# Performance work log

Hardware: AMD Instinct MI355X
Metric: run time of the kernel (lower is better)

## Reference

```python
import jax, jax.numpy as jnp
import numpy as np

NUM_ITERATIONS = 10
ALPHA = 0.1


def setup_inputs() -> dict:
    key = jax.random.key(0)
    k1, k2, k3, k4 = jax.random.split(key, 4)
    N, E, F_IN, H = 100000, 3200000, 512, 64
    x = jax.random.normal(k1, (N, F_IN), dtype=jnp.float32)
    edge_index = jax.random.randint(k2, (2, E), 0, N, dtype=jnp.int32)
    edge_weight = jnp.ones((E,), dtype=jnp.float32)
    # glorot-ish scaled dense weights
    W0 = jax.random.normal(k3, (F_IN, H), dtype=jnp.float32) * (2.0 / (F_IN + H)) ** 0.5
    b0 = jnp.zeros((H,), dtype=jnp.float32)
    W1 = jax.random.normal(k4, (H, H), dtype=jnp.float32) * (2.0 / (H + H)) ** 0.5
    b1 = jnp.zeros((H,), dtype=jnp.float32)
    return {"x": x, "edge_index": edge_index, "edge_weight": edge_weight,
            "W0": W0, "b0": b0, "W1": W1, "b1": b1}


def _gcn_norm_edge(edge_index, edge_weight, num_nodes):
    # renorm: add self-loops with weight 1, then symmetric D^-1/2 A D^-1/2
    row, col = edge_index[0], edge_index[1]
    loop = jnp.arange(num_nodes, dtype=edge_index.dtype)
    row = jnp.concatenate([row, loop])
    col = jnp.concatenate([col, loop])
    w = jnp.concatenate([edge_weight, jnp.ones((num_nodes,), edge_weight.dtype)])
    deg = jax.ops.segment_sum(w, row, num_segments=num_nodes)
    dinv = jnp.where(deg > 0, jax.lax.rsqrt(jnp.where(deg > 0, deg, 1.0)), 0.0)
    w_norm = dinv[row] * w * dinv[col]
    return row, col, w_norm


def reference(x, edge_index, edge_weight, W0, b0, W1, b1):
    N = x.shape[0]
    # MLP: hidden layers relu-activated, last layer unactivated
    h = jax.nn.relu(x @ W0 + b0)
    h = h @ W1 + b1  # [N, H]

    row, col, w_norm = _gcn_norm_edge(edge_index, edge_weight, N)

    def step(z, _):
        # sparse propagation: gather at source, weight, scatter-add at dest
        msg = z[row] * w_norm[:, None]                      # [E+N, H]
        agg = jax.ops.segment_sum(msg, col, num_segments=N)  # [N, H]
        return (1.0 - ALPHA) * agg + ALPHA * h, None

    z, _ = jax.lax.scan(step, h, None, length=NUM_ITERATIONS)
    return z
```

## Files before the change

### kernel.cpp

```cpp
#include <hip/hip_runtime.h>


#define PAGE 16128
#define BPP 64
#define XST 136

typedef __attribute__((ext_vector_type(8))) short bf16x8;
typedef __attribute__((ext_vector_type(4))) float f32x4;

__device__ __forceinline__ float bf_lo(unsigned z) { return __uint_as_float(z << 16); }
__device__ __forceinline__ float bf_hi(unsigned z) { return __uint_as_float(z & 0xffff0000u); }
__device__ __forceinline__ unsigned bf_rne(float x) {
    unsigned u = __float_as_uint(x);
    return (u + 0x7fffu + ((u >> 16) & 1u)) >> 16;
}
__device__ __forceinline__ unsigned bf_pack(float x, float y) { return bf_rne(x) | (bf_rne(y) << 16); }

__global__ __launch_bounds__(256) void k_deg(const int* __restrict__ row, const float* __restrict__ ew,
                                             float* __restrict__ slab, int E, int chunk) {
    __shared__ float hf[PAGE];
    int p = blockIdx.x / BPP, b = blockIdx.x - p * BPP;
    int lo = p * PAGE;
    for (int i = threadIdx.x; i < PAGE; i += 256) hf[i] = 0.f;
    __syncthreads();
    int e0 = b * chunk, e1 = min(e0 + chunk, E);
    int evec = e0 + ((e1 - e0) & ~3);
    for (int e = e0 + (int)threadIdx.x * 4; e + 4 <= evec; e += 1024) {
        int4 r4 = *(const int4*)(row + e);
        float4 w4 = *(const float4*)(ew + e);
        unsigned a = (unsigned)(r4.x - lo), bq = (unsigned)(r4.y - lo);
        unsigned c = (unsigned)(r4.z - lo), dq = (unsigned)(r4.w - lo);
        if (a < PAGE) atomicAdd(&hf[a], w4.x);
        if (bq < PAGE) atomicAdd(&hf[bq], w4.y);
        if (c < PAGE) atomicAdd(&hf[c], w4.z);
        if (dq < PAGE) atomicAdd(&hf[dq], w4.w);
    }
    for (int e = evec + (int)threadIdx.x; e < e1; e += 256) {
        unsigned a = (unsigned)(row[e] - lo);
        if (a < PAGE) atomicAdd(&hf[a], ew[e]);
    }
    __syncthreads();
    float* out = slab + (size_t)blockIdx.x * PAGE;
    for (int i = threadIdx.x; i < PAGE; i += 256) out[i] = hf[i];
}

__global__ __launch_bounds__(256) void k_fold_deg(const float* __restrict__ slab, float* __restrict__ dinv, int N) {
    int i = blockIdx.x * 256 + threadIdx.x;
    if (i >= N) return;
    int p = i / PAGE, ld = i - p * PAGE;
    const float* base = slab + (size_t)(p * BPP) * PAGE + ld;
    float d = 1.0f;
#pragma unroll
    for (int b = 0; b < BPP; ++b) d += base[(size_t)b * PAGE];
    dinv[i] = d > 0.f ? rsqrtf(d) : 0.f;
}

__global__ __launch_bounds__(256) void k_cnt(const int* __restrict__ col, unsigned short* __restrict__ slab,
                                             int E, int chunk) {
    __shared__ int hi[PAGE];
    int p = blockIdx.x / BPP, b = blockIdx.x - p * BPP;
    int lo = p * PAGE;
    for (int i = threadIdx.x; i < PAGE; i += 256) hi[i] = 0;
    __syncthreads();
    int e0 = b * chunk, e1 = min(e0 + chunk, E);
    int evec = e0 + ((e1 - e0) & ~3);
    for (int e = e0 + (int)threadIdx.x * 4; e + 4 <= evec; e += 1024) {
        int4 c4 = *(const int4*)(col + e);
        unsigned a = (unsigned)(c4.x - lo), bq = (unsigned)(c4.y - lo);
        unsigned c = (unsigned)(c4.z - lo), dq = (unsigned)(c4.w - lo);
        if (a < PAGE) atomicAdd(&hi[a], 1);
        if (bq < PAGE) atomicAdd(&hi[bq], 1);
        if (c < PAGE) atomicAdd(&hi[c], 1);
        if (dq < PAGE) atomicAdd(&hi[dq], 1);
    }
    for (int e = evec + (int)threadIdx.x; e < e1; e += 256) {
        unsigned a = (unsigned)(col[e] - lo);
        if (a < PAGE) atomicAdd(&hi[a], 1);
    }
    __syncthreads();
    unsigned short* out = slab + (size_t)blockIdx.x * PAGE;
    for (int i = threadIdx.x; i < PAGE; i += 256) out[i] = (unsigned short)hi[i];
}

__global__ __launch_bounds__(256) void k_fold_cnt(unsigned short* __restrict__ slab, int* __restrict__ cnt, int N) {
    int i = blockIdx.x * 256 + threadIdx.x;
    if (i >= N) return;
    int p = i / PAGE, ld = i - p * PAGE;
    unsigned short* base = slab + (size_t)(p * BPP) * PAGE + ld;
    int run = 0;
#pragma unroll
    for (int b = 0; b < BPP; ++b) {
        size_t off = (size_t)b * PAGE;
        int v = base[off];
        base[off] = (unsigned short)run;
        run += v;
    }
    cnt[i] = run;
}

__global__ __launch_bounds__(256) void k_scanA(const int* __restrict__ cnt, int* __restrict__ csum, int N) {
    __shared__ int s[256];
    int t = threadIdx.x, base = blockIdx.x * 1024;
    int p = 0;
#pragma unroll
    for (int j = 0; j < 4; ++j) { int idx = base + t + 256 * j; if (idx < N) p += cnt[idx]; }
    s[t] = p; __syncthreads();
    for (int off = 128; off > 0; off >>= 1) { if (t < off) s[t] += s[t + off]; __syncthreads(); }
    if (t == 0) csum[blockIdx.x] = s[0];
}

__global__ __launch_bounds__(256) void k_scanB(int* __restrict__ csum, int NC) {
    __shared__ int s[256];
    int t = threadIdx.x;
    int v = (t < NC) ? csum[t] : 0;
    s[t] = v; __syncthreads();
    for (int off = 1; off < 256; off <<= 1) {
        int x = (t >= off) ? s[t - off] : 0;
        __syncthreads();
        s[t] += x; __syncthreads();
    }
    if (t < NC) csum[t] = s[t] - v;
}

__global__ __launch_bounds__(256) void k_scanC(const int* __restrict__ cnt, const int* __restrict__ csum,
                                               int* __restrict__ rowp, int N) {
    __shared__ int s[256];
    int t = threadIdx.x, base = blockIdx.x * 1024 + t * 4;
    int c0 = (base + 0 < N) ? cnt[base + 0] : 0;
    int c1 = (base + 1 < N) ? cnt[base + 1] : 0;
    int c2 = (base + 2 < N) ? cnt[base + 2] : 0;
    int c3 = (base + 3 < N) ? cnt[base + 3] : 0;
    int ts = c0 + c1 + c2 + c3;
    s[t] = ts; __syncthreads();
    for (int off = 1; off < 256; off <<= 1) {
        int x = (t >= off) ? s[t - off] : 0;
        __syncthreads();
        s[t] += x; __syncthreads();
    }
    int o = csum[blockIdx.x] + s[t] - ts;
    if (base + 0 < N) rowp[base + 0] = o;
    if (base + 1 < N) rowp[base + 1] = o + c0;
    if (base + 2 < N) rowp[base + 2] = o + c0 + c1;
    if (base + 3 < N) rowp[base + 3] = o + c0 + c1 + c2;
}

__global__ __launch_bounds__(256) void k_scat(const int* __restrict__ row, const int* __restrict__ col,
                                              const float* __restrict__ ew, const float* __restrict__ dinv,
                                              const int* __restrict__ rowp, const unsigned short* __restrict__ slab,
                                              unsigned* __restrict__ srcw, int E, int chunk) {
    __shared__ int cur[PAGE];
    int p = blockIdx.x / BPP, b = blockIdx.x - p * BPP;
    int lo = p * PAGE;
    for (int i = threadIdx.x; i < PAGE; i += 256) cur[i] = 0;
    __syncthreads();
    const unsigned short* soff = slab + (size_t)blockIdx.x * PAGE;
    int e0 = b * chunk, e1 = min(e0 + chunk, E);
    int evec = e0 + ((e1 - e0) & ~3);
    for (int e = e0 + (int)threadIdx.x * 4; e + 4 <= evec; e += 1024) {
        int4 c4 = *(const int4*)(col + e);
        unsigned a = (unsigned)(c4.x - lo), bq = (unsigned)(c4.y - lo);
        unsigned cc = (unsigned)(c4.z - lo), dq = (unsigned)(c4.w - lo);
        if ((a < PAGE) | (bq < PAGE) | (cc < PAGE) | (dq < PAGE)) {
            int4 r4 = *(const int4*)(row + e);
            float4 w4 = *(const float4*)(ew + e);
            if (a < PAGE) {
                int pos = rowp[c4.x] + soff[a] + atomicAdd(&cur[a], 1);
                srcw[pos] = ((unsigned)r4.x << 15) | (bf_rne(dinv[r4.x] * w4.x) & 0x7fffu);
            }
            if (bq < PAGE) {
                int pos = rowp[c4.y] + soff[bq] + atomicAdd(&cur[bq], 1);
                srcw[pos] = ((unsigned)r4.y << 15) | (bf_rne(dinv[r4.y] * w4.y) & 0x7fffu);
            }
            if (cc < PAGE) {
                int pos = rowp[c4.z] + soff[cc] + atomicAdd(&cur[cc], 1);
                srcw[pos] = ((unsigned)r4.z << 15) | (bf_rne(dinv[r4.z] * w4.z) & 0x7fffu);
            }
            if (dq < PAGE) {
                int pos = rowp[c4.w] + soff[dq] + atomicAdd(&cur[dq], 1);
                srcw[pos] = ((unsigned)r4.w << 15) | (bf_rne(dinv[r4.w] * w4.w) & 0x7fffu);
            }
        }
    }
    for (int e = evec + (int)threadIdx.x; e < e1; e += 256) {
        int c = col[e];
        unsigned a = (unsigned)(c - lo);
        if (a < PAGE) {
            int r = row[e];
            int pos = rowp[c] + soff[a] + atomicAdd(&cur[a], 1);
            srcw[pos] = ((unsigned)r << 15) | (bf_rne(dinv[r] * ew[e]) & 0x7fffu);
        }
    }
}

__global__ __launch_bounds__(256) void k_wcvt(const float* __restrict__ W0, const float* __restrict__ W1,
                                              unsigned short* __restrict__ Th0, unsigned short* __restrict__ Tl0,
                                              unsigned short* __restrict__ Th1, unsigned short* __restrict__ Tl1) {
    int i = blockIdx.x * 256 + threadIdx.x;
    float v;
    unsigned short *th, *tl;
    size_t o;
    if (i < 512 * 64) {
        int k = i >> 6, n = i & 63;
        v = W0[i];
        th = Th0; tl = Tl0; o = (size_t)n * 512 + k;
    } else {
        int j = i - 512 * 64;
        if (j >= 64 * 64) return;
        int k = j >> 6, n = j & 63;
        v = W1[j];
        th = Th1; tl = Tl1; o = (size_t)n * 64 + k;
    }
    unsigned hi = bf_rne(v);
    float hv = __uint_as_float(hi << 16);
    unsigned lo = bf_rne(v - hv);
    th[o] = (unsigned short)hi;
    tl[o] = (unsigned short)lo;
}

__global__ __launch_bounds__(256, 4) void k_mlp(const float* __restrict__ x,
                                                const unsigned short* __restrict__ w0th, const unsigned short* __restrict__ w0tl,
                                                const unsigned short* __restrict__ w1th, const unsigned short* __restrict__ w1tl,
                                                const float* __restrict__ b0, const float* __restrict__ b1,
                                                unsigned* __restrict__ hb, int N) {
    __shared__ __align__(16) unsigned short xh[64 * XST];
    __shared__ __align__(16) unsigned short xl[64 * XST];
    int tid = threadIdx.x;
    int w = tid >> 6, lane = tid & 63;
    int g = lane >> 4, r16 = lane & 15;
    int rbase = blockIdx.x * 64;

    int r8 = tid >> 5;
    int c4 = tid & 31;
    const float* xbase = x + (size_t)(rbase + r8) * 512 + c4 * 4;

    auto LOADX = [&](float4 (&v)[8], int kc) {
#pragma unroll
        for (int i = 0; i < 8; ++i)
            v[i] = (rbase + i * 8 + r8 < N)
                       ? *(const float4*)(xbase + (size_t)i * 4096 + kc * 128)
                       : make_float4(0.f, 0.f, 0.f, 0.f);
    };
    auto CWRITE = [&](float4 (&v)[8]) {
#pragma unroll
        for (int i = 0; i < 8; ++i) {
            float e0 = v[i].x, e1 = v[i].y, e2 = v[i].z, e3 = v[i].w;
            unsigned u0 = __float_as_uint(e0), u1 = __float_as_uint(e1);
            unsigned u2 = __float_as_uint(e2), u3 = __float_as_uint(e3);
            unsigned short h0 = (unsigned short)(u0 >> 16), h1q = (unsigned short)(u1 >> 16);
            unsigned short h2 = (unsigned short)(u2 >> 16), h3 = (unsigned short)(u3 >> 16);
            float l0 = e0 - __uint_as_float(u0 & 0xffff0000u);
            float l1 = e1 - __uint_as_float(u1 & 0xffff0000u);
            float l2 = e2 - __uint_as_float(u2 & 0xffff0000u);
            float l3 = e3 - __uint_as_float(u3 & 0xffff0000u);
            int o = (i * 8 + r8) * XST + c4 * 4;
            ushort4 hv4 = make_ushort4(h0, h1q, h2, h3);
            ushort4 lv4 = make_ushort4((unsigned short)bf_rne(l0), (unsigned short)bf_rne(l1),
                                       (unsigned short)bf_rne(l2), (unsigned short)bf_rne(l3));
            *(ushort4*)(xh + o) = hv4;
            *(ushort4*)(xl + o) = lv4;
        }
    };

    f32x4 acc[4];
#pragma unroll
    for (int t = 0; t < 4; ++t) acc[t] = (f32x4){0.f, 0.f, 0.f, 0.f};

    float4 va[8], vb[8];
    LOADX(va, 0);
#pragma unroll
    for (int kc = 0; kc < 4; ++kc) {
        if (kc == 0) { if (0 < 3) LOADX(vb, 1); CWRITE(va); }
        else if (kc == 1) { LOADX(va, 2); CWRITE(vb); }
        else if (kc == 2) { LOADX(vb, 3); CWRITE(va); }
        else { CWRITE(vb); }
        __syncthreads();
#pragma unroll
        for (int ks = 0; ks < 4; ++ks) {
            int kk = ks * 32 + g * 8;
            bf16x8 ah = *(const bf16x8*)(xh + (w * 16 + r16) * XST + kk);
            bf16x8 al = *(const bf16x8*)(xl + (w * 16 + r16) * XST + kk);
            int kg = kc * 128 + kk;
#pragma unroll
            for (int t = 0; t < 4; ++t) {
                size_t wo = (size_t)(t * 16 + r16) * 512 + kg;
                bf16x8 wh = *(const bf16x8*)(w0th + wo);
                bf16x8 wl = *(const bf16x8*)(w0tl + wo);
                acc[t] = __builtin_amdgcn_mfma_f32_16x16x32_bf16(ah, wh, acc[t], 0, 0, 0);
                acc[t] = __builtin_amdgcn_mfma_f32_16x16x32_bf16(al, wh, acc[t], 0, 0, 0);
                acc[t] = __builtin_amdgcn_mfma_f32_16x16x32_bf16(ah, wl, acc[t], 0, 0, 0);
            }
        }
        __syncthreads();
    }
#pragma unroll
    for (int t = 0; t < 4; ++t) {
        int c = t * 16 + r16;
        float bb = b0[c];
#pragma unroll
        for (int r = 0; r < 4; ++r) {
            float vv = fmaxf(acc[t][r] + bb, 0.f);
            unsigned u = __float_as_uint(vv);
            unsigned short hi = (unsigned short)(u >> 16);
            float lo = vv - __uint_as_float(u & 0xffff0000u);
            int rr = w * 16 + g * 4 + r;
            xh[rr * 72 + c] = hi;
            xl[rr * 72 + c] = (unsigned short)bf_rne(lo);
        }
    }
    __syncthreads();
    f32x4 acc2[4];
#pragma unroll
    for (int t = 0; t < 4; ++t) acc2[t] = (f32x4){0.f, 0.f, 0.f, 0.f};
#pragma unroll
    for (int ks = 0; ks < 2; ++ks) {
        int k0 = ks * 32 + g * 8;
        bf16x8 ah = *(const bf16x8*)(xh + (w * 16 + r16) * 72 + k0);
        bf16x8 al = *(const bf16x8*)(xl + (w * 16 + r16) * 72 + k0);
#pragma unroll
        for (int t = 0; t < 4; ++t) {
            size_t wo = (size_t)(t * 16 + r16) * 64 + k0;
            bf16x8 wh = *(const bf16x8*)(w1th + wo);
            bf16x8 wl = *(const bf16x8*)(w1tl + wo);
            acc2[t] = __builtin_amdgcn_mfma_f32_16x16x32_bf16(ah, wh, acc2[t], 0, 0, 0);
            acc2[t] = __builtin_amdgcn_mfma_f32_16x16x32_bf16(al, wh, acc2[t], 0, 0, 0);
            acc2[t] = __builtin_amdgcn_mfma_f32_16x16x32_bf16(ah, wl, acc2[t], 0, 0, 0);
        }
    }
    unsigned short* hb16 = (unsigned short*)hb;
#pragma unroll
    for (int t = 0; t < 4; ++t) {
        int c = t * 16 + r16;
        float bb = b1[c];
#pragma unroll
        for (int r = 0; r < 4; ++r) {
            int grow = rbase + w * 16 + g * 4 + r;
            if (grow < N) {
                float vv = acc2[t][r] + bb;
                hb16[(size_t)grow * 64 + c] = (unsigned short)bf_rne(vv);
            }
        }
    }
}

__global__ __launch_bounds__(256) void k_prop(const unsigned* __restrict__ srcw,
                                              const int* __restrict__ rowp, const int* __restrict__ cnt,
                                              const float* __restrict__ dinv,
                                              const unsigned* __restrict__ zin, const unsigned* __restrict__ hb,
                                              unsigned* __restrict__ zout_b, float* __restrict__ zout_f, int N) {
    int wid = (blockIdx.x << 2) | (threadIdx.x >> 6);
    int d = __builtin_amdgcn_readfirstlane(wid);
    if (d >= N) return;
    int lane = threadIdx.x & 63;
    int half = lane >> 5, fi = lane & 31;
    int beg = rowp[d], end = beg + cnt[d];
    float ax = 0.f, ay = 0.f;
    for (int e = beg + half; e < end; e += 16) {
        unsigned pk[8];
#pragma unroll
        for (int k = 0; k < 8; ++k) {
            int idx = e + 2 * k;
            pk[k] = srcw[min(idx, end - 1)];
        }
        unsigned z[8];
#pragma unroll
        for (int k = 0; k < 8; ++k) z[k] = zin[(pk[k] >> 15) * 32u + fi];
#pragma unroll
        for (int k = 0; k < 8; ++k) {
            float w = (e + 2 * k < end) ? __uint_as_float((pk[k] & 0x7fffu) << 16) : 0.f;
            ax = fmaf(w, bf_lo(z[k]), ax);
            ay = fmaf(w, bf_hi(z[k]), ay);
        }
    }
    ax += __shfl_xor(ax, 32);
    ay += __shfl_xor(ay, 32);
    if (half == 0) {
        float di = dinv[d];
        unsigned zs = zin[(size_t)d * 32 + fi];
        float s2 = di * di;
        float ox = 0.9f * fmaf(di, ax, s2 * bf_lo(zs));
        float oy = 0.9f * fmaf(di, ay, s2 * bf_hi(zs));
        unsigned hz = hb[(size_t)d * 32 + fi];
        ox = fmaf(0.1f, bf_lo(hz), ox);
        oy = fmaf(0.1f, bf_hi(hz), oy);
        if (zout_f) ((float2*)zout_f)[(size_t)d * 32 + fi] = make_float2(ox, oy);
        else zout_b[(size_t)d * 32 + fi] = bf_pack(ox, oy);
    }
}

extern "C" void kernel_launch(void* const* d_in, const int* in_sizes, int n_in,
                              void* d_out, int out_size, void* d_ws, size_t ws_size,
                              hipStream_t stream) {
    const float* x  = (const float*)d_in[0];
    const int*   ei = (const int*)d_in[1];
    const float* ew = (const float*)d_in[2];
    const float* W0 = (const float*)d_in[3];
    const float* b0 = (const float*)d_in[4];
    const float* W1 = (const float*)d_in[5];
    const float* b1 = (const float*)d_in[6];
    int N = in_sizes[0] / 512;
    int E = in_sizes[2];
    const int* row = ei;
    const int* col = ei + E;

    char* p = (char*)d_ws;
    auto alloc = [&](size_t bytes) -> char* {
        char* r = p;
        p += (bytes + 255) & ~(size_t)255;
        return r;
    };
    int NPg = (N + PAGE - 1) / PAGE;
    size_t zbytes = (size_t)N * 32 * 4;
    size_t slab_bytes = (size_t)NPg * BPP * PAGE * 4;
    unsigned* hb  = (unsigned*)alloc(zbytes);
    float* slabf  = (float*)alloc(slab_bytes);
    unsigned* srcw = (unsigned*)alloc((size_t)E * 4);
    float* dinv  = (float*)alloc((size_t)N * 4);
    int* cnt     = (int*)alloc((size_t)N * 4);
    int* rowp    = (int*)alloc((size_t)N * 4);
    int* csum    = (int*)alloc(512 * 4);
    unsigned short* w0th = (unsigned short*)alloc(64 * 512 * 2);
    unsigned short* w0tl = (unsigned short*)alloc(64 * 512 * 2);
    unsigned short* w1th = (unsigned short*)alloc(64 * 64 * 2);
    unsigned short* w1tl = (unsigned short*)alloc(64 * 64 * 2);
    unsigned short* slabu = (unsigned short*)slabf;
    unsigned* zb0 = (unsigned*)slabf;
    unsigned* zb1 = (unsigned*)((char*)slabf + zbytes);

    int gN = (N + 255) / 256;
    int NC = (N + 1023) / 1024;
    int chunk = (((E + BPP - 1) / BPP) + 3) & ~3;
    int gridPg = NPg * BPP;

    k_wcvt<<<(512 * 64 + 64 * 64 + 255) / 256, 256, 0, stream>>>(W0, W1, w0th, w0tl, w1th, w1tl);
    k_deg<<<gridPg, 256, 0, stream>>>(row, ew, slabf, E, chunk);
    k_fold_deg<<<gN, 256, 0, stream>>>(slabf, dinv, N);
    k_cnt<<<gridPg, 256, 0, stream>>>(col, slabu, E, chunk);
    k_fold_cnt<<<gN, 256, 0, stream>>>(slabu, cnt, N);
    k_scanA<<<NC, 256, 0, stream>>>(cnt, csum, N);
    k_scanB<<<1, 256, 0, stream>>>(csum, NC);
    k_scanC<<<NC, 256, 0, stream>>>(cnt, csum, rowp, N);
    k_scat<<<gridPg, 256, 0, stream>>>(row, col, ew, dinv, rowp, slabu, srcw, E, chunk);
    k_mlp<<<(N + 63) / 64, 256, 0, stream>>>(x, w0th, w0tl, w1th, w1tl, b0, b1, hb, N);

    unsigned* zbufs[2] = { zb0, zb1 };
    const unsigned* zi = hb;
    int gP = (N + 3) / 4;
    for (int it = 0; it < 10; ++it) {
        if (it < 9) {
            unsigned* zo = zbufs[it & 1];
            k_prop<<<gP, 256, 0, stream>>>(srcw, rowp, cnt, dinv, zi, hb, zo, nullptr, N);
            zi = zo;
        } else {
            k_prop<<<gP, 256, 0, stream>>>(srcw, rowp, cnt, dinv, zi, hb, nullptr, (float*)d_out, N);
        }
    }
}
```

Before: 1.247 ms.

## Pre-swizzle MLP weights into MFMA fragment order and drop manual x double-buffer

Weight conversion now writes the hi/lo bf16 weights in a per-lane MFMA fragment order, with hi and lo adjacent. Each wave then loads weights with fully contiguous 16-byte-per-lane reads instead of strided row reads. The MLP kernel also drops its explicit register double-buffering of x tiles in favour of a simple load-convert loop, which lowers register pressure but exposes global load latency per chunk.

```diff
diff --git a/kernel.cpp b/kernel.cpp
--- a/kernel.cpp
+++ b/kernel.cpp
@@ -193,33 +193,38 @@
 }
 
 __global__ __launch_bounds__(256) void k_wcvt(const float* __restrict__ W0, const float* __restrict__ W1,
-                                              unsigned short* __restrict__ Th0, unsigned short* __restrict__ Tl0,
-                                              unsigned short* __restrict__ Th1, unsigned short* __restrict__ Tl1) {
-    int i = blockIdx.x * 256 + threadIdx.x;
-    float v;
-    unsigned short *th, *tl;
-    size_t o;
-    if (i < 512 * 64) {
-        int k = i >> 6, n = i & 63;
-        v = W0[i];
-        th = Th0; tl = Tl0; o = (size_t)n * 512 + k;
+                                              unsigned short* __restrict__ F0, unsigned short* __restrict__ F1) {
+    int o = blockIdx.x * 256 + threadIdx.x;
+    const float* W;
+    unsigned short* F;
+    int ksg, t, rem;
+    if (o < 64 * 512) {
+        int fragIdx = o >> 9;
+        rem = o & 511;
+        ksg = fragIdx >> 2; t = fragIdx & 3;
+        W = W0; F = F0 + (size_t)(fragIdx * 2) * 512;
     } else {
-        int j = i - 512 * 64;
-        if (j >= 64 * 64) return;
-        int k = j >> 6, n = j & 63;
-        v = W1[j];
-        th = Th1; tl = Tl1; o = (size_t)n * 64 + k;
-    }
+        int o2 = o - 64 * 512;
+        if (o2 >= 8 * 512) return;
+        int fragIdx = o2 >> 9;
+        rem = o2 & 511;
+        ksg = fragIdx >> 2; t = fragIdx & 3;
+        W = W1; F = F1 + (size_t)(fragIdx * 2) * 512;
+    }
+    int lane = rem >> 3, j = rem & 7;
+    int k = ksg * 32 + (lane >> 4) * 8 + j;
+    int n = t * 16 + (lane & 15);
+    float v = W[(size_t)k * 64 + n];
     unsigned hi = bf_rne(v);
     float hv = __uint_as_float(hi << 16);
     unsigned lo = bf_rne(v - hv);
-    th[o] = (unsigned short)hi;
-    tl[o] = (unsigned short)lo;
+    F[rem] = (unsigned short)hi;
+    F[512 + rem] = (unsigned short)lo;
 }
 
 __global__ __launch_bounds__(256, 4) void k_mlp(const float* __restrict__ x,
-                                                const unsigned short* __restrict__ w0th, const unsigned short* __restrict__ w0tl,
-                                                const unsigned short* __restrict__ w1th, const unsigned short* __restrict__ w1tl,
+                                                const unsigned short* __restrict__ w0f,
+                                                const unsigned short* __restrict__ w1f,
                                                 const float* __restrict__ b0, const float* __restrict__ b1,
                                                 unsigned* __restrict__ hb, int N) {
     __shared__ __align__(16) unsigned short xh[64 * XST];
@@ -233,14 +238,17 @@
     int c4 = tid & 31;
     const float* xbase = x + (size_t)(rbase + r8) * 512 + c4 * 4;
 
-    auto LOADX = [&](float4 (&v)[8], int kc) {
+    f32x4 acc[4];
+#pragma unroll
+    for (int t = 0; t < 4; ++t) acc[t] = (f32x4){0.f, 0.f, 0.f, 0.f};
+
+    for (int kc = 0; kc < 4; ++kc) {
+        float4 v[8];
 #pragma unroll
         for (int i = 0; i < 8; ++i)
             v[i] = (rbase + i * 8 + r8 < N)
                        ? *(const float4*)(xbase + (size_t)i * 4096 + kc * 128)
                        : make_float4(0.f, 0.f, 0.f, 0.f);
-    };
-    auto CWRITE = [&](float4 (&v)[8]) {
 #pragma unroll
         for (int i = 0; i < 8; ++i) {
             float e0 = v[i].x, e1 = v[i].y, e2 = v[i].z, e3 = v[i].w;
@@ -253,38 +261,22 @@
             float l2 = e2 - __uint_as_float(u2 & 0xffff0000u);
             float l3 = e3 - __uint_as_float(u3 & 0xffff0000u);
             int o = (i * 8 + r8) * XST + c4 * 4;
-            ushort4 hv4 = make_ushort4(h0, h1q, h2, h3);
-            ushort4 lv4 = make_ushort4((unsigned short)bf_rne(l0), (unsigned short)bf_rne(l1),
-                                       (unsigned short)bf_rne(l2), (unsigned short)bf_rne(l3));
-            *(ushort4*)(xh + o) = hv4;
-            *(ushort4*)(xl + o) = lv4;
-        }
-    };
-
-    f32x4 acc[4];
-#pragma unroll
-    for (int t = 0; t < 4; ++t) acc[t] = (f32x4){0.f, 0.f, 0.f, 0.f};
-
-    float4 va[8], vb[8];
-    LOADX(va, 0);
-#pragma unroll
-    for (int kc = 0; kc < 4; ++kc) {
-        if (kc == 0) { if (0 < 3) LOADX(vb, 1); CWRITE(va); }
-        else if (kc == 1) { LOADX(va, 2); CWRITE(vb); }
-        else if (kc == 2) { LOADX(vb, 3); CWRITE(va); }
-        else { CWRITE(vb); }
+            *(ushort4*)(xh + o) = make_ushort4(h0, h1q, h2, h3);
+            *(ushort4*)(xl + o) = make_ushort4((unsigned short)bf_rne(l0), (unsigned short)bf_rne(l1),
+                                               (unsigned short)bf_rne(l2), (unsigned short)bf_rne(l3));
+        }
         __syncthreads();
 #pragma unroll
         for (int ks = 0; ks < 4; ++ks) {
             int kk = ks * 32 + g * 8;
             bf16x8 ah = *(const bf16x8*)(xh + (w * 16 + r16) * XST + kk);
             bf16x8 al = *(const bf16x8*)(xl + (w * 16 + r16) * XST + kk);
-            int kg = kc * 128 + kk;
+            int ksg = kc * 4 + ks;
 #pragma unroll
             for (int t = 0; t < 4; ++t) {
-                size_t wo = (size_t)(t * 16 + r16) * 512 + kg;
-                bf16x8 wh = *(const bf16x8*)(w0th + wo);
-                bf16x8 wl = *(const bf16x8*)(w0tl + wo);
+                const unsigned short* wf = w0f + (size_t)((ksg * 4 + t) * 2) * 512 + lane * 8;
+                bf16x8 wh = *(const bf16x8*)wf;
+                bf16x8 wl = *(const bf16x8*)(wf + 512);
                 acc[t] = __builtin_amdgcn_mfma_f32_16x16x32_bf16(ah, wh, acc[t], 0, 0, 0);
                 acc[t] = __builtin_amdgcn_mfma_f32_16x16x32_bf16(al, wh, acc[t], 0, 0, 0);
                 acc[t] = __builtin_amdgcn_mfma_f32_16x16x32_bf16(ah, wl, acc[t], 0, 0, 0);
@@ -318,9 +310,9 @@
         bf16x8 al = *(const bf16x8*)(xl + (w * 16 + r16) * 72 + k0);
 #pragma unroll
         for (int t = 0; t < 4; ++t) {
-            size_t wo = (size_t)(t * 16 + r16) * 64 + k0;
-            bf16x8 wh = *(const bf16x8*)(w1th + wo);
-            bf16x8 wl = *(const bf16x8*)(w1tl + wo);
+            const unsigned short* wf = w1f + (size_t)((ks * 4 + t) * 2) * 512 + lane * 8;
+            bf16x8 wh = *(const bf16x8*)wf;
+            bf16x8 wl = *(const bf16x8*)(wf + 512);
             acc2[t] = __builtin_amdgcn_mfma_f32_16x16x32_bf16(ah, wh, acc2[t], 0, 0, 0);
             acc2[t] = __builtin_amdgcn_mfma_f32_16x16x32_bf16(al, wh, acc2[t], 0, 0, 0);
             acc2[t] = __builtin_amdgcn_mfma_f32_16x16x32_bf16(ah, wl, acc2[t], 0, 0, 0);
@@ -418,10 +410,8 @@
     int* cnt     = (int*)alloc((size_t)N * 4);
     int* rowp    = (int*)alloc((size_t)N * 4);
     int* csum    = (int*)alloc(512 * 4);
-    unsigned short* w0th = (unsigned short*)alloc(64 * 512 * 2);
-    unsigned short* w0tl = (unsigned short*)alloc(64 * 512 * 2);
-    unsigned short* w1th = (unsigned short*)alloc(64 * 64 * 2);
-    unsigned short* w1tl = (unsigned short*)alloc(64 * 64 * 2);
+    unsigned short* w0f = (unsigned short*)alloc(64 * 2 * 512 * 2);
+    unsigned short* w1f = (unsigned short*)alloc(8 * 2 * 512 * 2);
     unsigned short* slabu = (unsigned short*)slabf;
     unsigned* zb0 = (unsigned*)slabf;
     unsigned* zb1 = (unsigned*)((char*)slabf + zbytes);
@@ -431,7 +421,7 @@
     int chunk = (((E + BPP - 1) / BPP) + 3) & ~3;
     int gridPg = NPg * BPP;
 
-    k_wcvt<<<(512 * 64 + 64 * 64 + 255) / 256, 256, 0, stream>>>(W0, W1, w0th, w0tl, w1th, w1tl);
+    k_wcvt<<<(64 * 512 + 8 * 512 + 255) / 256, 256, 0, stream>>>(W0, W1, w0f, w1f);
     k_deg<<<gridPg, 256, 0, stream>>>(row, ew, slabf, E, chunk);
     k_fold_deg<<<gN, 256, 0, stream>>>(slabf, dinv, N);
     k_cnt<<<gridPg, 256, 0, stream>>>(col, slabu, E, chunk);
@@ -440,7 +430,7 @@
     k_scanB<<<1, 256, 0, stream>>>(csum, NC);
     k_scanC<<<NC, 256, 0, stream>>>(cnt, csum, rowp, N);
     k_scat<<<gridPg, 256, 0, stream>>>(row, col, ew, dinv, rowp, slabu, srcw, E, chunk);
-    k_mlp<<<(N + 63) / 64, 256, 0, stream>>>(x, w0th, w0tl, w1th, w1tl, b0, b1, hb, N);
+    k_mlp<<<(N + 63) / 64, 256, 0, stream>>>(x, w0f, w1f, b0, b1, hb, N);
 
     unsigned* zbufs[2] = { zb0, zb1 };
     const unsigned* zi = hb;
```

Result: faster. 1.175 ms (-5.7%).
